# Kernel tuning notes

Measured on AMD Instinct MI355X. Metric: run time of the kernel, lower is better.

The kernel has to match this reference:

```python
import jax, jax.numpy as jnp
import numpy as np
from jax import lax

B, C, T = 4, 512, 2304
H = 16
D = C // H          # 32 head dim
WIN = 19            # window_size
WOV = WIN // 2      # window_overlap = 9
W = 2 * WOV + 1     # band width = 19
EPS = 1e-5          # nn.LayerNorm default eps


def _dwconv(x, w):
    # depthwise Conv1d, kernel 3, pad 1, no bias, groups=C. x:[B,C,T], w:[C,1,3]
    return lax.conv_general_dilated(x, w, (1,), ((1, 1),),
                                    dimension_numbers=('NCH', 'OIH', 'NCH'),
                                    feature_group_count=C)


def _ln_c(x, g, b):
    # LayerNorm over channel dim of [B,C,T] (torch: permute->LN(n_embd)->permute)
    m = jnp.mean(x, axis=1, keepdims=True)
    v = jnp.var(x, axis=1, keepdims=True)
    return (x - m) * lax.rsqrt(v + EPS) * g[None, :, None] + b[None, :, None]


def _pw(x, w, b):
    # 1x1 Conv1d: [B,C,T] x [O,C] -> [B,O,T]
    return jnp.einsum('oc,bct->bot', w, x) + b[None, :, None]


def setup_inputs() -> dict:
    key = jax.random.key(0)
    ks = jax.random.split(key, 10)
    s = lambda shape, k, fan: jax.random.normal(k, shape, jnp.float32) * (1.0 / np.sqrt(fan))
    inp = {
        'x': jax.random.normal(ks[0], (B, C, T), jnp.float32),
        'w_qconv': s((C, 1, 3), ks[1], 3),
        'w_kconv': s((C, 1, 3), ks[2], 3),
        'w_vconv': s((C, 1, 3), ks[3], 3),
        'g_q': jnp.ones((C,), jnp.float32), 'b_q': jnp.zeros((C,), jnp.float32),
        'g_k': jnp.ones((C,), jnp.float32), 'b_k': jnp.zeros((C,), jnp.float32),
        'g_v': jnp.ones((C,), jnp.float32), 'b_v': jnp.zeros((C,), jnp.float32),
        'w_query': s((C, C), ks[4], C), 'b_query': jnp.zeros((C,), jnp.float32),
        'w_key': s((C, C), ks[5], C), 'b_key': jnp.zeros((C,), jnp.float32),
        'w_value': s((C, C), ks[6], C), 'b_value': jnp.zeros((C,), jnp.float32),
        'w_proj': s((C, C), ks[7], C), 'b_proj': jnp.zeros((C,), jnp.float32),
    }
    # realistic variable-length padding mask (valid prefix per sequence)
    lengths = jax.random.randint(ks[8], (B,), T // 2, T + 1)
    inp['mask'] = jnp.arange(T)[None, :] < lengths[:, None]  # [B,T] bool
    return inp


def reference(x, mask, w_qconv, w_kconv, w_vconv, g_q, b_q, g_k, b_k, g_v, b_v,
              w_query, b_query, w_key, b_key, w_value, b_value, w_proj, b_proj):
    mf = mask.astype(x.dtype)[:, None, :]  # [B,1,T]
    # depthwise conv QKV (+ mask) -> LayerNorm -> 1x1 projection
    q = _pw(_ln_c(_dwconv(x, w_qconv) * mf, g_q, b_q), w_query, b_query)
    k = _pw(_ln_c(_dwconv(x, w_kconv) * mf, g_k, b_k), w_key, b_key)
    v = _pw(_ln_c(_dwconv(x, w_vconv) * mf, g_v, b_v), w_value, b_value)
    # split heads: [B,C,T] -> [B,H,T,D] (channel layout C = H*D)
    split = lambda t: t.reshape(B, H, D, T).transpose(0, 1, 3, 2)
    q, k, v = split(q), split(k), split(v)
    scale = 1.0 / np.sqrt(D)
    # banded sliding-window attention: key position for (t, j) is t + j - WOV
    idx = jnp.arange(T)[:, None] + jnp.arange(W)[None, :]  # [T,W] indices into padded axis
    pad4 = lambda t: jnp.pad(t, ((0, 0), (0, 0), (WOV, WOV), (0, 0)))
    kg = pad4(k)[:, :, idx, :]  # [B,H,T,W,D]
    vg = pad4(v)[:, :, idx, :]  # [B,H,T,W,D]
    scores = jnp.einsum('bhtd,bhtwd->bhtw', q, kg) * scale  # [B,H,T,W]
    valid = (idx >= WOV) & (idx < T + WOV)  # in-range key positions [T,W]
    keym = jnp.pad(mask, ((0, 0), (WOV, WOV)))[:, idx]  # [B,T,W] kv padding mask
    addm = jnp.where(keym, 0.0, -1e4).astype(x.dtype)[:, None]  # additive -1e4 like torch
    scores = jnp.where(valid[None, None], scores + addm, -jnp.inf)
    probs = jax.nn.softmax(scores, axis=-1)
    probs = jnp.where(mask[:, None, :, None], probs, 0.0)  # zero masked query rows
    out = jnp.einsum('bhtw,bhtwd->bhtd', probs, vg)  # [B,H,T,D]
    out = out.transpose(0, 1, 3, 2).reshape(B, C, T)
    out = _pw(out, w_proj, b_proj) * mf
    return out, mask
```

## Files before the change

kernel.cpp:

```cpp
#include <hip/hip_runtime.h>
#include <cstdint>
#include <cstddef>

#define TB 4
#define TC 512
#define TT 2304
#define TH 16
#define TD 32
#define TW 19
#define WOVR 9
#define EPSLN 1e-5f
#define SCALE 0.17677669529663687f
#define MTOT (TB * TT)
#define KSZ  512

typedef __attribute__((ext_vector_type(8))) short s16x8;
typedef __attribute__((ext_vector_type(8))) unsigned short u16x8;
typedef __attribute__((ext_vector_type(4))) float f32x4;

__device__ __forceinline__ float bf2f(unsigned short u) {
  union { unsigned int i; float f; } x; x.i = ((unsigned int)u) << 16; return x.f;
}
__device__ __forceinline__ unsigned short f2bf(float f) {
  union { float f; unsigned int u; } x; x.f = f;
  unsigned int r = x.u + 0x7fffu + ((x.u >> 16) & 1u);
  return (unsigned short)(r >> 16);
}
__device__ __forceinline__ void gload16(const void* g, void* l) {
  __builtin_amdgcn_global_load_lds(
      (const __attribute__((address_space(1))) unsigned int*)g,
      (__attribute__((address_space(3))) unsigned int*)l, 16, 0, 0);
}

__global__ void k_prep(const unsigned char* __restrict__ mraw,
                       const float* __restrict__ wq, const float* __restrict__ wk,
                       const float* __restrict__ wv, const float* __restrict__ wp,
                       unsigned short* __restrict__ Wbf,
                       float* __restrict__ mf, float* __restrict__ out) {
  const int i = blockIdx.x * 256 + threadIdx.x;
  if (i < 4 * TC * TC) {
    const int z = i >> 18, r = i & (TC * TC - 1);
    const float* src = (z == 0) ? wq : (z == 1) ? wk : (z == 2) ? wv : wp;
    Wbf[i] = f2bf(src[r]);
  }
  if (i < TB * TT) {
    const uint32_t w0 = *(const uint32_t*)mraw;
    bool on;
    if (w0 == 1u)                 on = ((const int*)mraw)[i] != 0;
    else if (w0 == 0x01010101u)   on = mraw[i] != 0;
    else                          on = ((const float*)mraw)[i] != 0.0f;
    const float v = on ? 1.0f : 0.0f;
    mf[i] = v;
    out[(size_t)TB * TC * TT + i] = v;
  }
}

__global__ __launch_bounds__(512) void k_conv_ln_t(
    const float* __restrict__ x,
    const float* __restrict__ wq, const float* __restrict__ wk, const float* __restrict__ wv,
    const float* __restrict__ gq, const float* __restrict__ bq,
    const float* __restrict__ gk, const float* __restrict__ bk,
    const float* __restrict__ gv, const float* __restrict__ bv,
    const float* __restrict__ mf, unsigned short* __restrict__ Aall) {
  const int b = blockIdx.y;
  const int t0 = blockIdx.x * 16;
  const int tid = threadIdx.x;
  const int tt = tid & 15, cg = tid >> 4;
  const int tg = t0 + tt;
  const float m = mf[b * TT + tg];
  __shared__ float ps[3][32][16], ps2[3][32][16];
  __shared__ float mean_s[3][16], rstd_s[3][16];

  float s0 = 0.f, s20 = 0.f, s1 = 0.f, s21 = 0.f, s2v = 0.f, s22 = 0.f;
  unsigned int yp0[8], yp1[8], yp2[8];
  #pragma unroll
  for (int i = 0; i < 16; i++) {
    const int c = cg * 16 + i;
    const float* xp = x + ((size_t)(b * TC + c)) * TT + tg;
    const float xm1 = (tg > 0)      ? xp[-1] : 0.f;
    const float x0  = xp[0];
    const float xp1 = (tg < TT - 1) ? xp[1]  : 0.f;
    const float yq = (wq[c*3] * xm1 + wq[c*3+1] * x0 + wq[c*3+2] * xp1) * m;
    const float yk = (wk[c*3] * xm1 + wk[c*3+1] * x0 + wk[c*3+2] * xp1) * m;
    const float yv = (wv[c*3] * xm1 + wv[c*3+1] * x0 + wv[c*3+2] * xp1) * m;
    s0 += yq; s20 += yq * yq;
    s1 += yk; s21 += yk * yk;
    s2v += yv; s22 += yv * yv;
    const unsigned int hq = f2bf(yq), hk = f2bf(yk), hv = f2bf(yv);
    if ((i & 1) == 0) { yp0[i>>1] = hq; yp1[i>>1] = hk; yp2[i>>1] = hv; }
    else { yp0[i>>1] |= hq << 16; yp1[i>>1] |= hk << 16; yp2[i>>1] |= hv << 16; }
  }
  ps[0][cg][tt] = s0; ps2[0][cg][tt] = s20;
  ps[1][cg][tt] = s1; ps2[1][cg][tt] = s21;
  ps[2][cg][tt] = s2v; ps2[2][cg][tt] = s22;
  __syncthreads();
  if (tid < 48) {
    const int z = tid >> 4, tl = tid & 15;
    float su = 0.f, su2 = 0.f;
    #pragma unroll
    for (int g = 0; g < 32; g++) { su += ps[z][g][tl]; su2 += ps2[z][g][tl]; }
    const float mean = su * (1.f / TC);
    const float var  = su2 * (1.f / TC) - mean * mean;
    mean_s[z][tl] = mean;
    rstd_s[z][tl] = rsqrtf(fmaxf(var, 0.f) + EPSLN);
  }
  __syncthreads();

  #pragma unroll
  for (int z = 0; z < 3; z++) {
    const unsigned int* yp = (z == 0) ? yp0 : (z == 1) ? yp1 : yp2;
    const float* gp = (z == 0) ? gq : (z == 1) ? gk : gv;
    const float* bp = (z == 0) ? bq : (z == 1) ? bk : bv;
    const float mean = mean_s[z][tt], rs = rstd_s[z][tt];
    unsigned short tmp[16];
    #pragma unroll
    for (int i = 0; i < 16; i++) {
      const int c = cg * 16 + i;
      const unsigned short hb =
          (unsigned short)((i & 1) ? (yp[i>>1] >> 16) : (yp[i>>1] & 0xffffu));
      tmp[i] = f2bf((bf2f(hb) - mean) * rs * gp[c] + bp[c]);
    }
    unsigned short* oz = Aall + ((size_t)z * MTOT + b * TT + tg) * TC + cg * 16;
    *(u16x8*)(oz)     = *(const u16x8*)(tmp);
    *(u16x8*)(oz + 8) = *(const u16x8*)(tmp + 8);
  }
}

template<int F32OUT>
__global__ __launch_bounds__(256) void k_gemm_mfma(
    const unsigned short* __restrict__ Abase, const unsigned short* __restrict__ Wbase,
    const float* __restrict__ bq, const float* __restrict__ bk, const float* __restrict__ bv,
    unsigned short* __restrict__ obf, float* __restrict__ of32,
    const float* __restrict__ mf) {
  const int z = blockIdx.z;
  const unsigned short* A = Abase + (size_t)z * MTOT * KSZ;
  const unsigned short* W = Wbase + (size_t)z * KSZ * KSZ;
  const float* bias = (z == 0) ? bq : (z == 1) ? bk : bv;
  const int m0 = blockIdx.y * 128;
  const int n0 = blockIdx.x * 128;
  __shared__ __align__(16) unsigned short smem[4][128 * 32];
  const int tid = threadIdx.x;
  const int l = tid & 63, l15 = l & 15, l4 = l >> 4;
  const int wid = tid >> 6, wm = wid >> 1, wn = wid & 1;
  const int r0 = tid >> 2;
  const int c0 = (tid & 3) ^ ((r0 >> 1) & 3);
  const int r1 = r0 + 64;
  const int c1 = (tid & 3) ^ ((r1 >> 1) & 3);
  int offA[4], offB[4];
  #pragma unroll
  for (int i = 0; i < 4; i++) {
    int ra = wm * 64 + i * 16 + l15;
    offA[i] = (ra * 4 + (l4 ^ ((ra >> 1) & 3))) * 8;
    int rb = wn * 64 + i * 16 + l15;
    offB[i] = (rb * 4 + (l4 ^ ((rb >> 1) & 3))) * 8;
  }
  const size_t ga0 = (size_t)(m0 + r0) * KSZ + c0 * 8;
  const size_t ga1 = (size_t)(m0 + r1) * KSZ + c1 * 8;
  const size_t gb0 = (size_t)(n0 + r0) * KSZ + c0 * 8;
  const size_t gb1 = (size_t)(n0 + r1) * KSZ + c1 * 8;

  #define STAGE(buf, kk)                                            \
    do {                                                            \
      unsigned short* Ad = &smem[0][0] + (buf) * (128 * 32);        \
      unsigned short* Bd = &smem[2][0] + (buf) * (128 * 32);        \
      gload16(A + ga0 + (kk), Ad + tid * 8);                        \
      gload16(A + ga1 + (kk), Ad + (tid + 256) * 8);                \
      gload16(W + gb0 + (kk), Bd + tid * 8);                        \
      gload16(W + gb1 + (kk), Bd + (tid + 256) * 8);                \
    } while (0)

  f32x4 acc[4][4] = {};
  STAGE(0, 0);
  __syncthreads();
  int cur = 0;
  for (int k0 = 0; k0 < KSZ; k0 += 32) {
    if (k0 + 32 < KSZ) STAGE(cur ^ 1, k0 + 32);
    const unsigned short* Ac = &smem[0][0] + cur * (128 * 32);
    const unsigned short* Bc = &smem[2][0] + cur * (128 * 32);
    s16x8 av[4], bw[4];
    #pragma unroll
    for (int i = 0; i < 4; i++) {
      av[i] = *(const s16x8*)(Ac + offA[i]);
      bw[i] = *(const s16x8*)(Bc + offB[i]);
    }
    #pragma unroll
    for (int mi = 0; mi < 4; mi++)
      #pragma unroll
      for (int nj = 0; nj < 4; nj++)
        acc[mi][nj] = __builtin_amdgcn_mfma_f32_16x16x32_bf16(av[mi], bw[nj], acc[mi][nj], 0, 0, 0);
    __syncthreads();
    cur ^= 1;
  }
  #undef STAGE

  if (!F32OUT) {
    unsigned short* O = obf + (size_t)z * MTOT * KSZ;
    #pragma unroll
    for (int nj = 0; nj < 4; nj++) {
      const int col = n0 + wn * 64 + nj * 16 + l15;
      const float bi = bias[col];
      #pragma unroll
      for (int mi = 0; mi < 4; mi++) {
        const int mrow = m0 + wm * 64 + mi * 16 + l4 * 4;
        #pragma unroll
        for (int r = 0; r < 4; r++)
          O[(size_t)(mrow + r) * KSZ + col] = f2bf(acc[mi][nj][r] + bi);
      }
    }
  } else {
    const int bb = m0 / TT;
    const int tloc0 = m0 - bb * TT;
    float* tb = (float*)&smem[0][0];
    for (int c = 0; c < 4; c++) {
      if (wn == (c >> 1)) {
        #pragma unroll
        for (int njl = 0; njl < 2; njl++) {
          const int nj = (c & 1) * 2 + njl;
          const int col = n0 + wn * 64 + nj * 16 + l15;
          const float bi = bias[col];
          const int cl = njl * 16 + l15;
          #pragma unroll
          for (int mi = 0; mi < 4; mi++)
            #pragma unroll
            for (int r = 0; r < 4; r++)
              tb[cl * 132 + wm * 64 + mi * 16 + l4 * 4 + r] = acc[mi][nj][r] + bi;
        }
      }
      __syncthreads();
      const int ol = tid >> 3, part = tid & 7;
      const int o = n0 + c * 32 + ol;
      #pragma unroll
      for (int g = 0; g < 4; g++) {
        const int tl = part * 16 + g * 4;
        float4 v  = *(const float4*)&tb[ol * 132 + tl];
        float4 mm = *(const float4*)&mf[m0 + tl];
        v.x *= mm.x; v.y *= mm.y; v.z *= mm.z; v.w *= mm.w;
        *(float4*)&of32[((size_t)(bb * TC + o)) * TT + tloc0 + tl] = v;
      }
      __syncthreads();
    }
  }
}

#define AROWS (128 + 2 * WOVR)
#define ASTR  36
__global__ __launch_bounds__(256) void k_attn_lds(
    const unsigned short* __restrict__ QKV, const float* __restrict__ mf,
    unsigned short* __restrict__ AO) {
  const int t0 = blockIdx.x * 128;
  const int h = blockIdx.y, b = blockIdx.z;
  const int tid = threadIdx.x;
  const int tloc = tid >> 1, half = tid & 1;
  const size_t SZ = (size_t)MTOT * KSZ;
  const unsigned short* Qp = QKV;
  const unsigned short* Kp = QKV + SZ;
  const unsigned short* Vp = QKV + 2 * SZ;
  __shared__ unsigned short Ks[AROWS * ASTR], Vs[AROWS * ASTR];
  __shared__ float mfs[AROWS];

  for (int idx = tid; idx < 2 * AROWS * 4; idx += 256) {
    const int bufv = idx >= AROWS * 4;
    const int ci = idx - bufv * AROWS * 4;
    const int r = ci >> 2, c = ci & 3;
    const int tk = t0 - WOVR + r;
    const int tkc = tk < 0 ? 0 : (tk >= TT ? TT - 1 : tk);
    const unsigned short* src =
        (bufv ? Vp : Kp) + ((size_t)(b * TT + tkc)) * TC + h * TD + c * 8;
    uint4 v = *(const uint4*)src;
    unsigned short* dst = (bufv ? Vs : Ks) + r * ASTR + c * 8;
    uint2 lo; lo.x = v.x; lo.y = v.y;
    uint2 hi; hi.x = v.z; hi.y = v.w;
    *(uint2*)dst = lo; *(uint2*)(dst + 4) = hi;
  }
  if (tid < AROWS) {
    const int tk = t0 - WOVR + tid;
    mfs[tid] = (tk >= 0 && tk < TT) ? (mf[b * TT + tk] != 0.f ? 0.f : -1e4f)
                                    : -1e30f;
  }
  __syncthreads();

  const int t = t0 + tloc;
  const float qm = mf[b * TT + t];
  float q[16];
  {
    const unsigned short* qr = Qp + ((size_t)(b * TT + t)) * TC + h * TD + half * 16;
    #pragma unroll
    for (int c = 0; c < 2; c++) {
      u16x8 v = *(const u16x8*)(qr + c * 8);
      #pragma unroll
      for (int j = 0; j < 8; j++) q[c * 8 + j] = bf2f(v[j]);
    }
  }
  float e[TW];
  float smax = -3.0e38f;
  #pragma unroll
  for (int j = 0; j < TW; j++) {
    const unsigned short* kr = Ks + (tloc + j) * ASTR + half * 16;
    float acc = 0.f;
    #pragma unroll
    for (int c = 0; c < 4; c++) {
      uint2 w = *(const uint2*)(kr + c * 4);
      acc = fmaf(q[c*4+0], bf2f((unsigned short)(w.x & 0xffffu)), acc);
      acc = fmaf(q[c*4+1], bf2f((unsigned short)(w.x >> 16)), acc);
      acc = fmaf(q[c*4+2], bf2f((unsigned short)(w.y & 0xffffu)), acc);
      acc = fmaf(q[c*4+3], bf2f((unsigned short)(w.y >> 16)), acc);
    }
    acc += __shfl_xor(acc, 1, 64);
    const float sv = acc * SCALE + mfs[tloc + j];
    e[j] = sv;
    smax = fmaxf(smax, sv);
  }
  float den = 0.f;
  #pragma unroll
  for (int j = 0; j < TW; j++) { const float ev = __expf(e[j] - smax); e[j] = ev; den += ev; }
  float o[16] = {};
  #pragma unroll
  for (int j = 0; j < TW; j++) {
    const unsigned short* vr = Vs + (tloc + j) * ASTR + half * 16;
    const float p = e[j];
    #pragma unroll
    for (int c = 0; c < 4; c++) {
      uint2 w = *(const uint2*)(vr + c * 4);
      o[c*4+0] = fmaf(p, bf2f((unsigned short)(w.x & 0xffffu)), o[c*4+0]);
      o[c*4+1] = fmaf(p, bf2f((unsigned short)(w.x >> 16)), o[c*4+1]);
      o[c*4+2] = fmaf(p, bf2f((unsigned short)(w.y & 0xffffu)), o[c*4+2]);
      o[c*4+3] = fmaf(p, bf2f((unsigned short)(w.y >> 16)), o[c*4+3]);
    }
  }
  const float sc = qm / den;
  unsigned short tmp[16];
  #pragma unroll
  for (int i = 0; i < 16; i++) tmp[i] = f2bf(o[i] * sc);
  unsigned short* op = AO + ((size_t)(b * TT + t)) * TC + h * TD + half * 16;
  *(u16x8*)(op)     = *(const u16x8*)(tmp);
  *(u16x8*)(op + 8) = *(const u16x8*)(tmp + 8);
}

extern "C" void kernel_launch(void* const* d_in, const int* in_sizes, int n_in,
                              void* d_out, int out_size, void* d_ws, size_t ws_size,
                              hipStream_t stream) {
  const float* x       = (const float*)d_in[0];
  const float* w_qconv = (const float*)d_in[1];
  const float* w_kconv = (const float*)d_in[2];
  const float* w_vconv = (const float*)d_in[3];
  const float* g_q = (const float*)d_in[4];
  const float* b_q = (const float*)d_in[5];
  const float* g_k = (const float*)d_in[6];
  const float* b_k = (const float*)d_in[7];
  const float* g_v = (const float*)d_in[8];
  const float* b_v = (const float*)d_in[9];
  const float* w_query = (const float*)d_in[10];
  const float* b_query = (const float*)d_in[11];
  const float* w_key   = (const float*)d_in[12];
  const float* b_key   = (const float*)d_in[13];
  const float* w_value = (const float*)d_in[14];
  const float* b_value = (const float*)d_in[15];
  const float* w_proj  = (const float*)d_in[16];
  const float* b_proj  = (const float*)d_in[17];
  const unsigned char* mraw = (const unsigned char*)d_in[18];
  float* out = (float*)d_out;

  uint8_t* w8 = (uint8_t*)d_ws;
  float* mf            = (float*)w8;
  unsigned short* Wbf  = (unsigned short*)(w8 + (1ull << 20));
  unsigned short* Aall = (unsigned short*)(w8 + (4ull << 20));
  unsigned short* QKV  = (unsigned short*)(w8 + (34ull << 20));
  unsigned short* AO   = (unsigned short*)(w8 + (63ull << 20));

  k_prep<<<dim3((4 * TC * TC + 255) / 256), dim3(256), 0, stream>>>(
      mraw, w_query, w_key, w_value, w_proj, Wbf, mf, out);
  k_conv_ln_t<<<dim3(TT / 16, TB), dim3(512), 0, stream>>>(
      x, w_qconv, w_kconv, w_vconv, g_q, b_q, g_k, b_k, g_v, b_v, mf, Aall);
  k_gemm_mfma<0><<<dim3(4, MTOT / 128, 3), dim3(256), 0, stream>>>(
      Aall, Wbf, b_query, b_key, b_value, QKV, nullptr, mf);
  k_attn_lds<<<dim3(TT / 128, TH, TB), dim3(256), 0, stream>>>(QKV, mf, AO);
  k_gemm_mfma<1><<<dim3(4, MTOT / 128, 1), dim3(256), 0, stream>>>(
      AO, Wbf + 3 * TC * TC, b_proj, b_proj, b_proj, nullptr, out, mf);
}
```

Baseline: 109.4 us.

## Template GEMM on M tile, swap MFMA operands, and simplify epilogues

Result: no change. 110.5 us (+1.0%).

```diff
diff --git a/kernel.cpp b/kernel.cpp
--- a/kernel.cpp
+++ b/kernel.cpp
@@ -1,4 +1,5 @@
 #include <hip/hip_runtime.h>
+#include <hip/hip_bf16.h>
 #include <cstdint>
 #include <cstddef>
 
@@ -22,9 +23,9 @@
   union { unsigned int i; float f; } x; x.i = ((unsigned int)u) << 16; return x.f;
 }
 __device__ __forceinline__ unsigned short f2bf(float f) {
-  union { float f; unsigned int u; } x; x.f = f;
-  unsigned int r = x.u + 0x7fffu + ((x.u >> 16) & 1u);
-  return (unsigned short)(r >> 16);
+  union { __hip_bfloat16 h; unsigned short u; } c;
+  c.h = __float2bfloat16(f);
+  return c.u;
 }
 __device__ __forceinline__ void gload16(const void* g, void* l) {
   __builtin_amdgcn_global_load_lds(
@@ -126,68 +127,77 @@
   }
 }
 
-template<int F32OUT>
+template<int BM, int F32OUT>
 __global__ __launch_bounds__(256) void k_gemm_mfma(
     const unsigned short* __restrict__ Abase, const unsigned short* __restrict__ Wbase,
     const float* __restrict__ bq, const float* __restrict__ bk, const float* __restrict__ bv,
     unsigned short* __restrict__ obf, float* __restrict__ of32,
     const float* __restrict__ mf) {
+  constexpr int MI = BM / 32;
+  constexpr int QA = BM / 64;
+  constexpr int WROWS = BM / 2;
   const int z = blockIdx.z;
   const unsigned short* A = Abase + (size_t)z * MTOT * KSZ;
   const unsigned short* W = Wbase + (size_t)z * KSZ * KSZ;
   const float* bias = (z == 0) ? bq : (z == 1) ? bk : bv;
-  const int m0 = blockIdx.y * 128;
+  const int m0 = blockIdx.y * BM;
   const int n0 = blockIdx.x * 128;
-  __shared__ __align__(16) unsigned short smem[4][128 * 32];
+  __shared__ __align__(16) unsigned short smem[2 * (BM * 32) + 2 * (128 * 32)];
   const int tid = threadIdx.x;
   const int l = tid & 63, l15 = l & 15, l4 = l >> 4;
   const int wid = tid >> 6, wm = wid >> 1, wn = wid & 1;
-  const int r0 = tid >> 2;
-  const int c0 = (tid & 3) ^ ((r0 >> 1) & 3);
-  const int r1 = r0 + 64;
-  const int c1 = (tid & 3) ^ ((r1 >> 1) & 3);
-  int offA[4], offB[4];
-  #pragma unroll
-  for (int i = 0; i < 4; i++) {
-    int ra = wm * 64 + i * 16 + l15;
+
+  int offA[MI], offB[4];
+  #pragma unroll
+  for (int i = 0; i < MI; i++) {
+    const int ra = wm * WROWS + i * 16 + l15;
     offA[i] = (ra * 4 + (l4 ^ ((ra >> 1) & 3))) * 8;
-    int rb = wn * 64 + i * 16 + l15;
-    offB[i] = (rb * 4 + (l4 ^ ((rb >> 1) & 3))) * 8;
-  }
-  const size_t ga0 = (size_t)(m0 + r0) * KSZ + c0 * 8;
-  const size_t ga1 = (size_t)(m0 + r1) * KSZ + c1 * 8;
-  const size_t gb0 = (size_t)(n0 + r0) * KSZ + c0 * 8;
-  const size_t gb1 = (size_t)(n0 + r1) * KSZ + c1 * 8;
-
-  #define STAGE(buf, kk)                                            \
-    do {                                                            \
-      unsigned short* Ad = &smem[0][0] + (buf) * (128 * 32);        \
-      unsigned short* Bd = &smem[2][0] + (buf) * (128 * 32);        \
-      gload16(A + ga0 + (kk), Ad + tid * 8);                        \
-      gload16(A + ga1 + (kk), Ad + (tid + 256) * 8);                \
-      gload16(W + gb0 + (kk), Bd + tid * 8);                        \
-      gload16(W + gb1 + (kk), Bd + (tid + 256) * 8);                \
+  }
+  #pragma unroll
+  for (int j = 0; j < 4; j++) {
+    const int rb = wn * 64 + j * 16 + l15;
+    offB[j] = (rb * 4 + (l4 ^ ((rb >> 1) & 3))) * 8;
+  }
+
+  #define STAGE(buf, kk)                                                     \
+    do {                                                                     \
+      unsigned short* Ad = smem + (buf) * (BM * 32);                         \
+      unsigned short* Bd = smem + 2 * (BM * 32) + (buf) * (128 * 32);        \
+      _Pragma("unroll")                                                      \
+      for (int q = 0; q < QA; q++) {                                         \
+        const int row = q * 64 + (tid >> 2);                                 \
+        const int cc = (tid & 3) ^ ((row >> 1) & 3);                         \
+        gload16(A + (size_t)(m0 + row) * KSZ + (kk) + cc * 8,                \
+                Ad + (q * 256 + tid) * 8);                                   \
+      }                                                                      \
+      _Pragma("unroll")                                                      \
+      for (int q = 0; q < 2; q++) {                                          \
+        const int row = q * 64 + (tid >> 2);                                 \
+        const int cc = (tid & 3) ^ ((row >> 1) & 3);                         \
+        gload16(W + (size_t)(n0 + row) * KSZ + (kk) + cc * 8,                \
+                Bd + (q * 256 + tid) * 8);                                   \
+      }                                                                      \
     } while (0)
 
-  f32x4 acc[4][4] = {};
+  f32x4 acc[MI][4] = {};
   STAGE(0, 0);
   __syncthreads();
   int cur = 0;
   for (int k0 = 0; k0 < KSZ; k0 += 32) {
     if (k0 + 32 < KSZ) STAGE(cur ^ 1, k0 + 32);
-    const unsigned short* Ac = &smem[0][0] + cur * (128 * 32);
-    const unsigned short* Bc = &smem[2][0] + cur * (128 * 32);
-    s16x8 av[4], bw[4];
-    #pragma unroll
-    for (int i = 0; i < 4; i++) {
-      av[i] = *(const s16x8*)(Ac + offA[i]);
-      bw[i] = *(const s16x8*)(Bc + offB[i]);
-    }
-    #pragma unroll
-    for (int mi = 0; mi < 4; mi++)
+    const unsigned short* Ac = smem + cur * (BM * 32);
+    const unsigned short* Bc = smem + 2 * (BM * 32) + cur * (128 * 32);
+    s16x8 av[MI], bw[4];
+    #pragma unroll
+    for (int i = 0; i < MI; i++) av[i] = *(const s16x8*)(Ac + offA[i]);
+    #pragma unroll
+    for (int j = 0; j < 4; j++)  bw[j] = *(const s16x8*)(Bc + offB[j]);
+    #pragma unroll
+    for (int mi = 0; mi < MI; mi++)
       #pragma unroll
       for (int nj = 0; nj < 4; nj++)
-        acc[mi][nj] = __builtin_amdgcn_mfma_f32_16x16x32_bf16(av[mi], bw[nj], acc[mi][nj], 0, 0, 0);
+        acc[mi][nj] = __builtin_amdgcn_mfma_f32_16x16x32_bf16(
+            bw[nj], av[mi], acc[mi][nj], 0, 0, 0);
     __syncthreads();
     cur ^= 1;
   }
@@ -197,47 +207,40 @@
     unsigned short* O = obf + (size_t)z * MTOT * KSZ;
     #pragma unroll
     for (int nj = 0; nj < 4; nj++) {
-      const int col = n0 + wn * 64 + nj * 16 + l15;
-      const float bi = bias[col];
+      const int ch0 = n0 + wn * 64 + nj * 16 + l4 * 4;
+      const float4 bi = *(const float4*)&bias[ch0];
       #pragma unroll
-      for (int mi = 0; mi < 4; mi++) {
-        const int mrow = m0 + wm * 64 + mi * 16 + l4 * 4;
-        #pragma unroll
-        for (int r = 0; r < 4; r++)
-          O[(size_t)(mrow + r) * KSZ + col] = f2bf(acc[mi][nj][r] + bi);
+      for (int mi = 0; mi < MI; mi++) {
+        const int bt = m0 + wm * WROWS + mi * 16 + l15;
+        const float v0 = acc[mi][nj][0] + bi.x;
+        const float v1 = acc[mi][nj][1] + bi.y;
+        const float v2 = acc[mi][nj][2] + bi.z;
+        const float v3 = acc[mi][nj][3] + bi.w;
+        uint2 pk;
+        pk.x = (uint32_t)f2bf(v0) | ((uint32_t)f2bf(v1) << 16);
+        pk.y = (uint32_t)f2bf(v2) | ((uint32_t)f2bf(v3) << 16);
+        *(uint2*)&O[(size_t)bt * KSZ + ch0] = pk;
       }
     }
   } else {
     const int bb = m0 / TT;
-    const int tloc0 = m0 - bb * TT;
-    float* tb = (float*)&smem[0][0];
-    for (int c = 0; c < 4; c++) {
-      if (wn == (c >> 1)) {
+    const int tl0 = m0 - bb * TT;
+    #pragma unroll
+    for (int mi = 0; mi < MI; mi++) {
+      const int bt = m0 + wm * WROWS + mi * 16 + l15;
+      const int tloc = tl0 + wm * WROWS + mi * 16 + l15;
+      const float mm = mf[bt];
+      #pragma unroll
+      for (int nj = 0; nj < 4; nj++) {
+        const int ch0 = n0 + wn * 64 + nj * 16 + l4 * 4;
+        const float4 bi = *(const float4*)&bias[ch0];
         #pragma unroll
-        for (int njl = 0; njl < 2; njl++) {
-          const int nj = (c & 1) * 2 + njl;
-          const int col = n0 + wn * 64 + nj * 16 + l15;
-          const float bi = bias[col];
-          const int cl = njl * 16 + l15;
-          #pragma unroll
-          for (int mi = 0; mi < 4; mi++)
-            #pragma unroll
-            for (int r = 0; r < 4; r++)
-              tb[cl * 132 + wm * 64 + mi * 16 + l4 * 4 + r] = acc[mi][nj][r] + bi;
+        for (int r = 0; r < 4; r++) {
+          const float biv = r == 0 ? bi.x : r == 1 ? bi.y : r == 2 ? bi.z : bi.w;
+          of32[((size_t)(bb * TC + ch0 + r)) * TT + tloc] =
+              (acc[mi][nj][r] + biv) * mm;
         }
       }
-      __syncthreads();
-      const int ol = tid >> 3, part = tid & 7;
-      const int o = n0 + c * 32 + ol;
-      #pragma unroll
-      for (int g = 0; g < 4; g++) {
-        const int tl = part * 16 + g * 4;
-        float4 v  = *(const float4*)&tb[ol * 132 + tl];
-        float4 mm = *(const float4*)&mf[m0 + tl];
-        v.x *= mm.x; v.y *= mm.y; v.z *= mm.z; v.w *= mm.w;
-        *(float4*)&of32[((size_t)(bb * TC + o)) * TT + tloc0 + tl] = v;
-      }
-      __syncthreads();
     }
   }
 }
@@ -371,9 +374,9 @@
       mraw, w_query, w_key, w_value, w_proj, Wbf, mf, out);
   k_conv_ln_t<<<dim3(TT / 16, TB), dim3(512), 0, stream>>>(
       x, w_qconv, w_kconv, w_vconv, g_q, b_q, g_k, b_k, g_v, b_v, mf, Aall);
-  k_gemm_mfma<0><<<dim3(4, MTOT / 128, 3), dim3(256), 0, stream>>>(
+  k_gemm_mfma<256, 0><<<dim3(4, MTOT / 256, 3), dim3(256), 0, stream>>>(
       Aall, Wbf, b_query, b_key, b_value, QKV, nullptr, mf);
   k_attn_lds<<<dim3(TT / 128, TH, TB), dim3(256), 0, stream>>>(QKV, mf, AO);
-  k_gemm_mfma<1><<<dim3(4, MTOT / 128, 1), dim3(256), 0, stream>>>(
+  k_gemm_mfma<128, 1><<<dim3(4, MTOT / 128, 1), dim3(256), 0, stream>>>(
       AO, Wbf + 3 * TC * TC, b_proj, b_proj, b_proj, nullptr, out, mf);
 }
```
